# Performance work log

Measured on AMD Instinct MI355X. Metric: run time of the kernel, lower is better.

The kernel has to match this reference:

```python
import jax, jax.numpy as jnp
import numpy as np

D = 64; H = 8; HD = 8; L = 3; FFN = 256
MAX_CHUNKS = 1024; MCL = 16


def rms_norm(x, w, eps=1e-6):
    return x * w * jax.lax.rsqrt(jnp.mean(x * x, axis=-1, keepdims=True) + eps)


def rope(x):
    # x: [B, S, H, HD]
    S, hd = x.shape[1], x.shape[-1]
    half = hd // 2
    freqs = 1.0 / (10000.0 ** (jnp.arange(half, dtype=x.dtype) * 2.0 / hd))
    ang = jnp.arange(S, dtype=x.dtype)[:, None] * freqs  # [S, half]
    cos = jnp.cos(ang)[None, :, None, :]
    sin = jnp.sin(ang)[None, :, None, :]
    x1, x2 = x[..., :half], x[..., half:]
    return jnp.concatenate([x1 * cos - x2 * sin, x1 * sin + x2 * cos], axis=-1)


def block(x, wq, wk, wv, wo, g1, g2, w1, w2):
    B, S, _ = x.shape
    h = rms_norm(x, g1)
    q = rope((h @ wq).reshape(B, S, H, HD))
    k = rope((h @ wk).reshape(B, S, H, HD))
    v = (h @ wv).reshape(B, S, H, HD)
    scores = jnp.einsum('bqhd,bkhd->bhqk', q, k) / jnp.sqrt(jnp.asarray(HD, x.dtype))
    causal = jnp.tril(jnp.ones((S, S), dtype=bool))
    scores = jnp.where(causal, scores, jnp.asarray(-1e30, x.dtype))
    attn = jax.nn.softmax(scores, axis=-1)
    o = jnp.einsum('bhqk,bkhd->bqhd', attn, v).reshape(B, S, D)
    x = x + o @ wo
    h2 = rms_norm(x, g2)
    return x + jax.nn.gelu(h2 @ w1, approximate=False) @ w2


def setup_inputs() -> dict:
    key = jax.random.key(0)
    ks = jax.random.split(key, 12)
    B, S = 4, 2048
    s = 1.0 / np.sqrt(D)
    return {
        'x': jax.random.normal(ks[0], (B, S, D), jnp.float32),
        'pad_token_vector': jax.random.normal(ks[1], (D,), jnp.float32),
        'x_ids': jax.random.randint(ks[2], (B, S), 0, 256),
        'pad_token_id': 257,
        'Wq': jax.random.normal(ks[3], (L, D, D), jnp.float32) * s,
        'Wk': jax.random.normal(ks[4], (L, D, D), jnp.float32) * s,
        'Wv': jax.random.normal(ks[5], (L, D, D), jnp.float32) * s,
        'Wo': jax.random.normal(ks[6], (L, D, D), jnp.float32) * s,
        'ln1': jnp.ones((L, D), jnp.float32),
        'ln2': jnp.ones((L, D), jnp.float32),
        'W1': jax.random.normal(ks[7], (L, D, FFN), jnp.float32) * s,
        'W2': jax.random.normal(ks[8], (L, FFN, D), jnp.float32) * (1.0 / np.sqrt(FFN)),
        'Whead': jax.random.normal(ks[9], (D, 2), jnp.float32) * s,
        'bhead': jnp.zeros((2,), jnp.float32),
    }


def reference(x, pad_token_vector, x_ids, pad_token_id, Wq, Wk, Wv, Wo, ln1, ln2, W1, W2, Whead, bhead):
    B, S, _ = x.shape
    h = x
    for l in range(L):
        h = block(h, Wq[l], Wk[l], Wv[l], Wo[l], ln1[l], ln2[l], W1[l], W2[l])
    logits = h @ Whead + bhead  # [B, S, 2]
    end_mask = logits[..., 0] > logits[..., 1]  # [B, S]
    t = jnp.arange(S)
    # fallback: if a row has no end, mark the last position as an end
    has_end = jnp.any(end_mask, axis=-1, keepdims=True)
    end_mask = jnp.where(has_end, end_mask, t[None, :] == S - 1)
    em = end_mask.astype(jnp.int32)
    num_ends = jnp.sum(em, axis=-1)                 # [B] = number of chunks
    chunk_id = jnp.cumsum(em, axis=-1) - em         # exclusive count of prior ends
    prev_end = jnp.concatenate([jnp.ones((B, 1), bool), end_mask[:, :-1]], axis=1)
    start_marker = jnp.where(prev_end, t[None, :], -1)
    start = jax.lax.associative_scan(jnp.maximum, start_marker, axis=-1)  # cummax -> chunk start per token
    pos = t[None, :] - start                        # position within chunk
    valid = (chunk_id < num_ends[:, None]) & (chunk_id < MAX_CHUNKS) & (pos < MCL)
    c_idx = jnp.where(valid, chunk_id, MAX_CHUNKS)  # invalid -> dummy chunk, sliced off
    p_idx = jnp.where(valid, pos, 0)
    b_idx = jnp.arange(B)[:, None]
    out = jnp.broadcast_to(pad_token_vector, (B, MAX_CHUNKS + 1, MCL, D))
    out = out.at[b_idx, c_idx, p_idx].set(h)[:, :MAX_CHUNKS]
    ids = jnp.full((B, MAX_CHUNKS + 1, MCL), pad_token_id, dtype=x_ids.dtype)
    ids = ids.at[b_idx, c_idx, p_idx].set(x_ids)[:, :MAX_CHUNKS]
    reg_term = jnp.mean(logits[..., 1])
    return out, ids, reg_term
```

## Files before the change

kernel.cpp:

```cpp
#include <hip/hip_runtime.h>
#include <math.h>

constexpr int D   = 64;
constexpr int H   = 8;
constexpr int HD  = 8;
constexpr int NL  = 3;
constexpr int FFNx= 256;
constexpr int Bb  = 4;
constexpr int Ss  = 2048;
constexpr int NT  = Bb * Ss;
constexpr int MAXC= 1024;
constexpr int MCL = 16;

constexpr int TPB  = 72;
constexpr int BPB  = 36;
constexpr int PBSZ = 2304;

constexpr size_t WX  = 0;
constexpr size_t WQ  = 524288;
constexpr size_t WKV = 2621440;
constexpr size_t WPB = 4194304;
constexpr size_t WL1 = 9764864;
constexpr size_t WEM = WL1 + NT;
constexpr size_t WINV= WEM + NT;
constexpr size_t WCT = WINV + Bb*MAXC*MCL;
constexpr size_t WST = WCT + Ss*4;

constexpr float LOG2E = 1.4426950408889634f;

typedef float v2f  __attribute__((ext_vector_type(2)));
typedef float f16v __attribute__((ext_vector_type(16)));
using ckv_t = const __attribute__((address_space(4))) f16v*;

__device__ __forceinline__ float rdlane(float v, int l) {
    return __builtin_bit_cast(float, __builtin_amdgcn_readlane(__builtin_bit_cast(int, v), l));
}

__global__ void k_init(const float* __restrict__ x, float* __restrict__ X,
                       float* __restrict__ ct, float* __restrict__ st) {
    int i = blockIdx.x * blockDim.x + threadIdx.x;
    constexpr int N4 = NT * D / 4;
    if (i < N4) ((float4*)X)[i] = ((const float4*)x)[i];
    if (i < Ss * 4) {
        int s = i >> 2, f = i & 3;
        const float fr[4] = {1.0f, 0.1f, 0.01f, 0.001f};
        float ang = (float)s * fr[f];
        ct[i] = cosf(ang);
        st[i] = sinf(ang);
    }
}

__global__ __launch_bounds__(256) void k_qkv(
    const float* __restrict__ X, const float* __restrict__ Wq,
    const float* __restrict__ Wk, const float* __restrict__ Wv,
    const float* __restrict__ g1, const float* __restrict__ ct,
    const float* __restrict__ st, float* __restrict__ Q,
    float* __restrict__ KV) {
    __shared__ float wq_s[D*D], wk_s[D*D], wv_s[D*D];
    __shared__ float g_s[D];
    int tid = threadIdx.x;
    for (int i = tid; i < D*D; i += 256) {
        wq_s[i] = Wq[i]; wk_s[i] = Wk[i]; wv_s[i] = Wv[i];
    }
    if (tid < D) g_s[tid] = g1[tid];
    __syncthreads();
    int w = tid >> 6, d = tid & 63;
    int t0 = blockIdx.x * 16;
    for (int it = 0; it < 4; ++it) {
        int t = t0 + it*4 + w;
        float xv = X[t*D + d];
        float ss = xv * xv;
        #pragma unroll
        for (int off = 32; off; off >>= 1) ss += __shfl_xor(ss, off);
        float r = 1.0f / sqrtf(ss * (1.0f/D) + 1e-6f);
        float h = xv * g_s[d] * r;
        float aq = 0.f, ak = 0.f, av = 0.f;
        #pragma unroll
        for (int j = 0; j < D; ++j) {
            float hj = rdlane(h, j);
            aq += hj * wq_s[j*D + d];
            ak += hj * wk_s[j*D + d];
            av += hj * wv_s[j*D + d];
        }
        int s  = t & (Ss - 1);
        int e  = d & 7;
        int fi = e & 3;
        float c  = ct[s*4 + fi];
        float sn = st[s*4 + fi];
        float pq = __shfl_xor(aq, 4);
        float pk = __shfl_xor(ak, 4);
        float rq, rk;
        if (e < 4) { rq = aq*c - pq*sn; rk = ak*c - pk*sn; }
        else       { rq = pq*sn + aq*c; rk = pk*sn + ak*c; }
        Q[t*D + d] = rq;
        int bq = t >> 11;
        int hh = d >> 3;
        float* kvp = KV + ((((size_t)(bq*H + hh))*Ss + s) << 4);
        kvp[e]     = rk;
        kvp[8 + e] = av;
    }
}

template<int DIAG>
__device__ __forceinline__ void attn_loop4(
    ckv_t kvs, int L, int rel0,
    const v2f* __restrict__ qp0, const v2f* __restrict__ qp1,
    v2f& l0, v2f& l1, v2f* __restrict__ o0, v2f* __restrict__ o1) {
    #pragma unroll 4
    for (int j = 0; j < 64; ++j) {
        f16v kv = kvs[j];
        v2f a1;
        a1  = qp1[0] * (v2f){kv[0], kv[0]};
        a1 += qp1[1] * (v2f){kv[1], kv[1]};
        a1 += qp1[2] * (v2f){kv[2], kv[2]};
        a1 += qp1[3] * (v2f){kv[3], kv[3]};
        a1 += qp1[4] * (v2f){kv[4], kv[4]};
        a1 += qp1[5] * (v2f){kv[5], kv[5]};
        a1 += qp1[6] * (v2f){kv[6], kv[6]};
        a1 += qp1[7] * (v2f){kv[7], kv[7]};
        if (DIAG == 2) {
            int rel = rel0 + j;
            if (rel > L)      a1.x = -1e30f;
            if (rel > L + 64) a1.y = -1e30f;
        }
        v2f p1;
        p1.x = __builtin_amdgcn_exp2f(a1.x);
        p1.y = __builtin_amdgcn_exp2f(a1.y);
        l1 += p1;
        o1[0] += p1 * (v2f){kv[8],  kv[8]};
        o1[1] += p1 * (v2f){kv[9],  kv[9]};
        o1[2] += p1 * (v2f){kv[10], kv[10]};
        o1[3] += p1 * (v2f){kv[11], kv[11]};
        o1[4] += p1 * (v2f){kv[12], kv[12]};
        o1[5] += p1 * (v2f){kv[13], kv[13]};
        o1[6] += p1 * (v2f){kv[14], kv[14]};
        o1[7] += p1 * (v2f){kv[15], kv[15]};
        if (DIAG != 2) {
            v2f a0;
            a0  = qp0[0] * (v2f){kv[0], kv[0]};
            a0 += qp0[1] * (v2f){kv[1], kv[1]};
            a0 += qp0[2] * (v2f){kv[2], kv[2]};
            a0 += qp0[3] * (v2f){kv[3], kv[3]};
            a0 += qp0[4] * (v2f){kv[4], kv[4]};
            a0 += qp0[5] * (v2f){kv[5], kv[5]};
            a0 += qp0[6] * (v2f){kv[6], kv[6]};
            a0 += qp0[7] * (v2f){kv[7], kv[7]};
            if (DIAG == 1) {
                int rel = rel0 + j;
                if (rel > L)      a0.x = -1e30f;
                if (rel > L + 64) a0.y = -1e30f;
            }
            v2f p0;
            p0.x = __builtin_amdgcn_exp2f(a0.x);
            p0.y = __builtin_amdgcn_exp2f(a0.y);
            l0 += p0;
            o0[0] += p0 * (v2f){kv[8],  kv[8]};
            o0[1] += p0 * (v2f){kv[9],  kv[9]};
            o0[2] += p0 * (v2f){kv[10], kv[10]};
            o0[3] += p0 * (v2f){kv[11], kv[11]};
            o0[4] += p0 * (v2f){kv[12], kv[12]};
            o0[5] += p0 * (v2f){kv[13], kv[13]};
            o0[6] += p0 * (v2f){kv[14], kv[14]};
            o0[7] += p0 * (v2f){kv[15], kv[15]};
        }
    }
}

__global__ __launch_bounds__(256) void k_attn2(
    const float* __restrict__ Qg, const float* __restrict__ KV,
    float* __restrict__ PB) {
    __shared__ float comb[2][PBSZ];
    int xcd  = blockIdx.x & 7;
    int slot = blockIdx.x >> 3;
    int bhg  = slot / BPB;
    int blk  = slot - bhg * BPB;
    int bh   = bhg * 8 + xcd;
    int wvu  = __builtin_amdgcn_readfirstlane(threadIdx.x >> 6);
    int pair = wvu >> 1;
    int half = wvu & 1;
    int widb = blk * 2 + pair;
    int L = threadIdx.x & 63;
    int rem = widb;
    int s = 0;
    while (rem >= 8 - (s >> 1)) { rem -= 8 - (s >> 1); ++s; }
    int t = (s >> 1) + rem;
    int b = bh >> 3, h = bh & 7;
    int qmin = t * 256;
    int k0 = s * 128 + half * 64;

    const float SC = 0.35355339059327373f * LOG2E;
    const float* qp = Qg + ((size_t)(b*Ss + qmin + L))*D + h*HD;
    float4 qa0 = *(const float4*)(qp);
    float4 qb0 = *(const float4*)(qp + 4);
    float4 qa1 = *(const float4*)(qp + 64*D);
    float4 qb1 = *(const float4*)(qp + 64*D + 4);
    float4 qa2 = *(const float4*)(qp + 128*D);
    float4 qb2 = *(const float4*)(qp + 128*D + 4);
    float4 qa3 = *(const float4*)(qp + 192*D);
    float4 qb3 = *(const float4*)(qp + 192*D + 4);
    v2f qp0[8], qp1[8];
    qp0[0] = (v2f){qa0.x*SC, qa1.x*SC};  qp1[0] = (v2f){qa2.x*SC, qa3.x*SC};
    qp0[1] = (v2f){qa0.y*SC, qa1.y*SC};  qp1[1] = (v2f){qa2.y*SC, qa3.y*SC};
    qp0[2] = (v2f){qa0.z*SC, qa1.z*SC};  qp1[2] = (v2f){qa2.z*SC, qa3.z*SC};
    qp0[3] = (v2f){qa0.w*SC, qa1.w*SC};  qp1[3] = (v2f){qa2.w*SC, qa3.w*SC};
    qp0[4] = (v2f){qb0.x*SC, qb1.x*SC};  qp1[4] = (v2f){qb2.x*SC, qb3.x*SC};
    qp0[5] = (v2f){qb0.y*SC, qb1.y*SC};  qp1[5] = (v2f){qb2.y*SC, qb3.y*SC};
    qp0[6] = (v2f){qb0.z*SC, qb1.z*SC};  qp1[6] = (v2f){qb2.z*SC, qb3.z*SC};
    qp0[7] = (v2f){qb0.w*SC, qb1.w*SC};  qp1[7] = (v2f){qb2.w*SC, qb3.w*SC};

    v2f l0 = (v2f){0.f, 0.f}, l1 = (v2f){0.f, 0.f};
    v2f o0[8], o1[8];
    #pragma unroll
    for (int e = 0; e < 8; ++e) { o0[e] = (v2f){0.f, 0.f}; o1[e] = (v2f){0.f, 0.f}; }

    ckv_t kvs = (ckv_t)(unsigned long long)(KV + (((size_t)bh*Ss + k0) << 4));
    if (s == 2*t)          attn_loop4<1>(kvs, L, half*64, qp0, qp1, l0, l1, o0, o1);
    else if (s == 2*t + 1) attn_loop4<2>(kvs, L, half*64, qp0, qp1, l0, l1, o0, o1);
    else                   attn_loop4<0>(kvs, L, half*64, qp0, qp1, l0, l1, o0, o1);

    if (half == 1) {
        comb[pair][L]       = l0.x;
        comb[pair][64 + L]  = l0.y;
        comb[pair][128 + L] = l1.x;
        comb[pair][192 + L] = l1.y;
        #pragma unroll
        for (int e = 0; e < 8; ++e) {
            comb[pair][256 + e*256 + L]       = o0[e].x;
            comb[pair][256 + e*256 + 64 + L]  = o0[e].y;
            comb[pair][256 + e*256 + 128 + L] = o1[e].x;
            comb[pair][256 + e*256 + 192 + L] = o1[e].y;
        }
    }
    __syncthreads();
    if (half == 0) {
        int pbidx = t*(t+1) + s;
        float* pb = PB + ((size_t)bh * TPB + pbidx) * PBSZ;
        pb[L]       = l0.x + comb[pair][L];
        pb[64 + L]  = l0.y + comb[pair][64 + L];
        pb[128 + L] = l1.x + comb[pair][128 + L];
        pb[192 + L] = l1.y + comb[pair][192 + L];
        #pragma unroll
        for (int e = 0; e < 8; ++e) {
            pb[256 + e*256 + L]       = o0[e].x + comb[pair][256 + e*256 + L];
            pb[256 + e*256 + 64 + L]  = o0[e].y + comb[pair][256 + e*256 + 64 + L];
            pb[256 + e*256 + 128 + L] = o1[e].x + comb[pair][256 + e*256 + 128 + L];
            pb[256 + e*256 + 192 + L] = o1[e].y + comb[pair][256 + e*256 + 192 + L];
        }
    }
}

__global__ __launch_bounds__(256) void k_combo(
    const float* __restrict__ PB, float* __restrict__ X,
    const float* __restrict__ Wo) {
    __shared__ float wo_s[D*D];
    __shared__ float oT[32][65];
    int tid = threadIdx.x;
    int seg = blockIdx.x & 7;
    int t   = (blockIdx.x >> 3) & 7;
    int b   = blockIdx.x >> 6;
    for (int i = tid; i < D*D; i += 256) wo_s[i] = Wo[i];

    int h  = tid >> 5;
    int ql = tid & 31;
    int qs = seg*32 + ql;
    int bh = b*8 + h;
    int nch = 2*(t+1);
    float Lx = 0.f;
    float O[8] = {0,0,0,0,0,0,0,0};
    for (int s3 = 0; s3 < nch; ++s3) {
        int idx = t*(t+1) + s3;
        const float* pb = PB + (size_t)(bh*TPB + idx) * PBSZ;
        Lx += pb[qs];
        #pragma unroll
        for (int e = 0; e < 8; ++e) O[e] += pb[256 + e*256 + qs];
    }
    float inv = 1.0f / Lx;
    #pragma unroll
    for (int e = 0; e < 8; ++e) oT[ql][h*8 + e] = O[e] * inv;
    __syncthreads();

    int d = tid & 63, wv = tid >> 6;
    #pragma unroll 2
    for (int k = 0; k < 8; ++k) {
        int tt = wv*8 + k;
        float a = 0.f;
        #pragma unroll
        for (int j = 0; j < D; ++j) a += oT[tt][j] * wo_s[j*D + d];
        X[((size_t)(b*Ss) + t*256 + seg*32 + tt)*D + d] += a;
    }
}

template<bool HEAD>
__global__ __launch_bounds__(256) void k_ffn(
    float* __restrict__ X, const float* __restrict__ g2,
    const float* __restrict__ W1, const float* __restrict__ W2,
    const float* __restrict__ Wh, const float* __restrict__ bhp,
    float* __restrict__ logit1, int* __restrict__ em) {
    __shared__ __align__(16) float h2t[64][20];
    __shared__ float part[16][16];
    __shared__ float g_s[D];
    __shared__ __align__(16) float ult[FFNx][20];
    __shared__ float red[4][16][D];
    int tid = threadIdx.x;
    if (tid < D) g_s[tid] = g2[tid];
    int t0 = blockIdx.x * 16;
    int tk = tid >> 4, li = tid & 15;
    float x0 = X[(t0+tk)*D + li];
    float x1 = X[(t0+tk)*D + li + 16];
    float x2 = X[(t0+tk)*D + li + 32];
    float x3 = X[(t0+tk)*D + li + 48];
    part[tk][li] = x0*x0 + x1*x1 + x2*x2 + x3*x3;
    __syncthreads();
    if (tid < 16) {
        float s = 0.f;
        #pragma unroll
        for (int i = 0; i < 16; ++i) s += part[tid][i];
        part[tid][0] = 1.0f / sqrtf(s * (1.0f/D) + 1e-6f);
    }
    __syncthreads();
    float r = part[tk][0];
    h2t[li][tk]      = x0 * g_s[li]      * r;
    h2t[li + 16][tk] = x1 * g_s[li + 16] * r;
    h2t[li + 32][tk] = x2 * g_s[li + 32] * r;
    h2t[li + 48][tk] = x3 * g_s[li + 48] * r;
    __syncthreads();
    {
        int f = tid;
        v2f acc2[8];
        #pragma unroll
        for (int i = 0; i < 8; ++i) acc2[i] = (v2f){0.f, 0.f};
        for (int j = 0; j < D; ++j) {
            float wv = W1[j*FFNx + f];
            v2f wv2 = (v2f){wv, wv};
            const float4* hp = (const float4*)&h2t[j][0];
            float4 a0 = hp[0], a1 = hp[1], a2 = hp[2], a3 = hp[3];
            const v2f* a0v = (const v2f*)&a0;
            const v2f* a1v = (const v2f*)&a1;
            const v2f* a2v = (const v2f*)&a2;
            const v2f* a3v = (const v2f*)&a3;
            acc2[0] += a0v[0]*wv2;  acc2[1] += a0v[1]*wv2;
            acc2[2] += a1v[0]*wv2;  acc2[3] += a1v[1]*wv2;
            acc2[4] += a2v[0]*wv2;  acc2[5] += a2v[1]*wv2;
            acc2[6] += a3v[0]*wv2;  acc2[7] += a3v[1]*wv2;
        }
        #pragma unroll
        for (int i = 0; i < 8; ++i) {
            float ua = acc2[i].x;
            float ub = acc2[i].y;
            ua = 0.5f * ua * (1.0f + erff(ua * 0.70710678118654752f));
            ub = 0.5f * ub * (1.0f + erff(ub * 0.70710678118654752f));
            ult[f][2*i]     = ua;
            ult[f][2*i + 1] = ub;
        }
    }
    __syncthreads();
    {
        int d = tid & 63, fp = tid >> 6;
        v2f acc2[8];
        #pragma unroll
        for (int i = 0; i < 8; ++i) acc2[i] = (v2f){0.f, 0.f};
        for (int fo = 0; fo < 64; ++fo) {
            int f = fp*64 + fo;
            float wv = W2[f*D + d];
            v2f wv2 = (v2f){wv, wv};
            const float4* up = (const float4*)&ult[f][0];
            float4 u0 = up[0], u1 = up[1], u2 = up[2], u3 = up[3];
            const v2f* u0v = (const v2f*)&u0;
            const v2f* u1v = (const v2f*)&u1;
            const v2f* u2v = (const v2f*)&u2;
            const v2f* u3v = (const v2f*)&u3;
            acc2[0] += u0v[0]*wv2;  acc2[1] += u0v[1]*wv2;
            acc2[2] += u1v[0]*wv2;  acc2[3] += u1v[1]*wv2;
            acc2[4] += u2v[0]*wv2;  acc2[5] += u2v[1]*wv2;
            acc2[6] += u3v[0]*wv2;  acc2[7] += u3v[1]*wv2;
        }
        #pragma unroll
        for (int i = 0; i < 8; ++i) {
            red[fp][2*i][d]     = acc2[i].x;
            red[fp][2*i + 1][d] = acc2[i].y;
        }
        __syncthreads();
        int tk2 = tid >> 6;
        #pragma unroll
        for (int k = 0; k < 4; ++k) {
            int tt = tk2 + k*4;
            float sum = red[0][tt][d] + red[1][tt][d] + red[2][tt][d] + red[3][tt][d];
            float xf = X[(t0 + tt)*D + d] + sum;
            X[(t0 + tt)*D + d] = xf;
            if (HEAD) {
                float p0 = xf * Wh[d*2];
                float p1 = xf * Wh[d*2 + 1];
                #pragma unroll
                for (int off = 32; off; off >>= 1) {
                    p0 += __shfl_xor(p0, off);
                    p1 += __shfl_xor(p1, off);
                }
                if (d == 0) {
                    float l0 = p0 + bhp[0], l1 = p1 + bhp[1];
                    em[t0 + tt] = (l0 > l1) ? 1 : 0;
                    logit1[t0 + tt] = l1;
                }
            }
        }
    }
}

__global__ __launch_bounds__(256) void k_scanreg(
    const int* __restrict__ em, int* __restrict__ inv,
    const float* __restrict__ logit1, float* __restrict__ outreg) {
    __shared__ int ssum[256], smax[256];
    __shared__ int sany, stot;
    int tid = threadIdx.x;
    if (blockIdx.x == Bb) {
        __shared__ float redf[256];
        float s = 0.f;
        for (int i = tid; i < NT; i += 256) s += logit1[i];
        redf[tid] = s;
        __syncthreads();
        for (int off = 128; off; off >>= 1) {
            if (tid < off) redf[tid] += redf[tid + off];
            __syncthreads();
        }
        if (tid == 0) *outreg = redf[0] * (1.0f / NT);
        return;
    }
    int b = blockIdx.x;
    int* invb = inv + b * (MAXC*MCL);
    for (int i = tid; i < MAXC*MCL; i += 256) invb[i] = -1;
    __syncthreads();
    const int* e = em + b*Ss;
    int base = tid * 8;
    int loc[8];
    int lsum = 0, lor = 0;
    #pragma unroll
    for (int i = 0; i < 8; ++i) { loc[i] = e[base + i]; lsum += loc[i]; lor |= loc[i]; }
    ssum[tid] = lor;
    __syncthreads();
    if (tid == 0) { int a = 0; for (int i = 0; i < 256; ++i) a |= ssum[i]; sany = a; }
    __syncthreads();
    int any = sany;
    __syncthreads();
    if (!any && tid == 255) { loc[7] = 1; lsum = 1; }
    int prev = (tid == 0) ? 1 : e[base - 1];
    if (!any && tid) prev = 0;
    int mk[8];
    int lmax = -1;
    #pragma unroll
    for (int i = 0; i < 8; ++i) {
        int pe = (i == 0) ? prev : loc[i - 1];
        if (i == 7 && !any && tid == 255) pe = e[base + 6];
        mk[i] = pe ? (base + i) : -1;
        lmax = max(lmax, mk[i]);
    }
    ssum[tid] = lsum; smax[tid] = lmax;
    __syncthreads();
    if (tid == 0) {
        int rs = 0, rm = -1;
        for (int i = 0; i < 256; ++i) {
            int ts = ssum[i], tm = smax[i];
            ssum[i] = rs; smax[i] = rm;
            rs += ts; rm = max(rm, tm);
        }
        stot = rs;
    }
    __syncthreads();
    int run = ssum[tid], rmax = smax[tid], tot = stot;
    #pragma unroll
    for (int i = 0; i < 8; ++i) {
        int s = base + i;
        rmax = max(rmax, mk[i]);
        int chunk = run;
        run += loc[i];
        int pos = s - rmax;
        bool valid = (chunk < tot) && (chunk < MAXC) && (pos < MCL);
        if (valid) invb[chunk * MCL + pos] = b*Ss + s;
    }
}

__global__ __launch_bounds__(256) void k_out(
    const float* __restrict__ X, const float* __restrict__ pad,
    const int* __restrict__ xids, const int* __restrict__ padid,
    const int* __restrict__ inv, float* __restrict__ out) {
    int i = blockIdx.x * blockDim.x + threadIdx.x;
    constexpr int NV4 = Bb * MAXC * MCL * D / 4;
    constexpr int NI4 = Bb * MAXC * MCL / 4;
    if (i < NV4) {
        int slot = i >> 4;
        int d4 = i & 15;
        int t = inv[slot];
        float4 v = (t >= 0) ? ((const float4*)X)[t*16 + d4]
                            : ((const float4*)pad)[d4];
        ((float4*)out)[i] = v;
    } else if (i < NV4 + NI4) {
        int j = i - NV4;
        float pv = (float)(*padid);
        int base = j * 4;
        int t0_ = inv[base], t1_ = inv[base+1], t2_ = inv[base+2], t3_ = inv[base+3];
        float4 v;
        v.x = (t0_ >= 0) ? (float)xids[t0_] : pv;
        v.y = (t1_ >= 0) ? (float)xids[t1_] : pv;
        v.z = (t2_ >= 0) ? (float)xids[t2_] : pv;
        v.w = (t3_ >= 0) ? (float)xids[t3_] : pv;
        ((float4*)out)[i] = v;
    }
}

extern "C" void kernel_launch(void* const* d_in, const int* in_sizes, int n_in,
                              void* d_out, int out_size, void* d_ws, size_t ws_size,
                              hipStream_t stream) {
    const float* x    = (const float*)d_in[0];
    const float* pad  = (const float*)d_in[1];
    const int*   xids = (const int*)  d_in[2];
    const int*   padid= (const int*)  d_in[3];
    const float* Wq   = (const float*)d_in[4];
    const float* Wk   = (const float*)d_in[5];
    const float* Wv   = (const float*)d_in[6];
    const float* Wo   = (const float*)d_in[7];
    const float* ln1  = (const float*)d_in[8];
    const float* ln2  = (const float*)d_in[9];
    const float* W1   = (const float*)d_in[10];
    const float* W2   = (const float*)d_in[11];
    const float* Wh   = (const float*)d_in[12];
    const float* bh   = (const float*)d_in[13];
    float* out = (float*)d_out;
    float* ws  = (float*)d_ws;

    float* X  = ws + WX;
    float* Qb = ws + WQ;
    float* KVb= ws + WKV;
    float* PBb= ws + WPB;
    float* L1b= ws + WL1;
    int*   EMb= (int*)(ws + WEM);
    int*   INVb=(int*)(ws + WINV);
    float* ct = ws + WCT;
    float* st = ws + WST;

    k_init<<<2048, 256, 0, stream>>>(x, X, ct, st);
    for (int l = 0; l < NL; ++l) {
        k_qkv <<<512, 256, 0, stream>>>(X, Wq + l*D*D, Wk + l*D*D, Wv + l*D*D,
                                        ln1 + l*D, ct, st, Qb, KVb);
        k_attn2<<<32*BPB, 256, 0, stream>>>(Qb, KVb, PBb);
        k_combo<<<256, 256, 0, stream>>>(PBb, X, Wo + l*D*D);
        if (l == NL - 1)
            k_ffn<true ><<<NT/16, 256, 0, stream>>>(X, ln2 + l*D, W1 + l*D*FFNx,
                                                    W2 + l*FFNx*D, Wh, bh, L1b, EMb);
        else
            k_ffn<false><<<NT/16, 256, 0, stream>>>(X, ln2 + l*D, W1 + l*D*FFNx,
                                                    W2 + l*FFNx*D, nullptr, nullptr,
                                                    nullptr, nullptr);
    }
    k_scanreg<<<Bb + 1, 256, 0, stream>>>(EMb, INVb, L1b,
                                          out + (size_t)Bb*MAXC*MCL*D + Bb*MAXC*MCL);
    k_out <<<(Bb*MAXC*MCL*D/4 + Bb*MAXC*MCL/4 + 255)/256, 256, 0, stream>>>(
        X, pad, xids, padid, INVb, out);
}
```

Baseline: 273.8 us.

## Fuse attention partial combine and output projection into the FFN kernel

Merges k_combo (combining the partial attention blocks, normalising, and applying Wo plus the residual) into the FFN kernel. Each block now handles 16 tokens and keeps the updated residual in shared memory, so X is not written and then re-read between the two stages, and one launch per layer goes away. In exchange every block of the 512 reloads the full Wo matrix (previously 256 blocks did), and shared-memory use per block grows, which may lower occupancy.

```diff
diff --git a/kernel.cpp b/kernel.cpp
--- a/kernel.cpp
+++ b/kernel.cpp
@@ -249,66 +249,69 @@
     }
 }
 
-__global__ __launch_bounds__(256) void k_combo(
+template<bool HEAD>
+__global__ __launch_bounds__(256) void k_cffn(
     const float* __restrict__ PB, float* __restrict__ X,
-    const float* __restrict__ Wo) {
-    __shared__ float wo_s[D*D];
-    __shared__ float oT[32][65];
-    int tid = threadIdx.x;
-    int seg = blockIdx.x & 7;
-    int t   = (blockIdx.x >> 3) & 7;
-    int b   = blockIdx.x >> 6;
-    for (int i = tid; i < D*D; i += 256) wo_s[i] = Wo[i];
-
-    int h  = tid >> 5;
-    int ql = tid & 31;
-    int qs = seg*32 + ql;
-    int bh = b*8 + h;
-    int nch = 2*(t+1);
-    float Lx = 0.f;
-    float O[8] = {0,0,0,0,0,0,0,0};
-    for (int s3 = 0; s3 < nch; ++s3) {
-        int idx = t*(t+1) + s3;
-        const float* pb = PB + (size_t)(bh*TPB + idx) * PBSZ;
-        Lx += pb[qs];
-        #pragma unroll
-        for (int e = 0; e < 8; ++e) O[e] += pb[256 + e*256 + qs];
-    }
-    float inv = 1.0f / Lx;
-    #pragma unroll
-    for (int e = 0; e < 8; ++e) oT[ql][h*8 + e] = O[e] * inv;
-    __syncthreads();
-
-    int d = tid & 63, wv = tid >> 6;
-    #pragma unroll 2
-    for (int k = 0; k < 8; ++k) {
-        int tt = wv*8 + k;
-        float a = 0.f;
-        #pragma unroll
-        for (int j = 0; j < D; ++j) a += oT[tt][j] * wo_s[j*D + d];
-        X[((size_t)(b*Ss) + t*256 + seg*32 + tt)*D + d] += a;
-    }
-}
-
-template<bool HEAD>
-__global__ __launch_bounds__(256) void k_ffn(
-    float* __restrict__ X, const float* __restrict__ g2,
+    const float* __restrict__ Wo, const float* __restrict__ g2,
     const float* __restrict__ W1, const float* __restrict__ W2,
     const float* __restrict__ Wh, const float* __restrict__ bhp,
     float* __restrict__ logit1, int* __restrict__ em) {
+    __shared__ float wo_s[D*D];
+    __shared__ float oT[16][65];
+    __shared__ float xt[16][65];
     __shared__ __align__(16) float h2t[64][20];
     __shared__ float part[16][16];
     __shared__ float g_s[D];
     __shared__ __align__(16) float ult[FFNx][20];
     __shared__ float red[4][16][D];
     int tid = threadIdx.x;
+    int gb  = blockIdx.x;
+    int b    = gb >> 7;
+    int tile = gb & 127;
+    int t    = tile >> 4;
+    int sq   = (tile & 15) << 4;
+    int tok0 = b*Ss + t*256 + sq;
+    for (int i = tid; i < D*D; i += 256) wo_s[i] = Wo[i];
     if (tid < D) g_s[tid] = g2[tid];
-    int t0 = blockIdx.x * 16;
+
+    {
+        int h  = tid >> 5;
+        int ql = (tid >> 1) & 15;
+        int eh = tid & 1;
+        int qs = sq + ql;
+        int bh = b*8 + h;
+        int nch = 2*(t+1);
+        float Lx = 0.f;
+        float O[4] = {0,0,0,0};
+        for (int s3 = 0; s3 < nch; ++s3) {
+            int idx = t*(t+1) + s3;
+            const float* pb = PB + (size_t)(bh*TPB + idx) * PBSZ;
+            Lx += pb[qs];
+            #pragma unroll
+            for (int e = 0; e < 4; ++e) O[e] += pb[256 + (eh*4 + e)*256 + qs];
+        }
+        float inv = 1.0f / Lx;
+        #pragma unroll
+        for (int e = 0; e < 4; ++e) oT[ql][h*8 + eh*4 + e] = O[e] * inv;
+    }
+    __syncthreads();
+    {
+        int d = tid & 63, wv = tid >> 6;
+        #pragma unroll
+        for (int k = 0; k < 4; ++k) {
+            int tt = wv*4 + k;
+            float a = 0.f;
+            #pragma unroll
+            for (int j = 0; j < D; ++j) a += oT[tt][j] * wo_s[j*D + d];
+            xt[tt][d] = X[(size_t)(tok0 + tt)*D + d] + a;
+        }
+    }
+    __syncthreads();
     int tk = tid >> 4, li = tid & 15;
-    float x0 = X[(t0+tk)*D + li];
-    float x1 = X[(t0+tk)*D + li + 16];
-    float x2 = X[(t0+tk)*D + li + 32];
-    float x3 = X[(t0+tk)*D + li + 48];
+    float x0 = xt[tk][li];
+    float x1 = xt[tk][li + 16];
+    float x2 = xt[tk][li + 32];
+    float x3 = xt[tk][li + 48];
     part[tk][li] = x0*x0 + x1*x1 + x2*x2 + x3*x3;
     __syncthreads();
     if (tid < 16) {
@@ -385,8 +388,8 @@
         for (int k = 0; k < 4; ++k) {
             int tt = tk2 + k*4;
             float sum = red[0][tt][d] + red[1][tt][d] + red[2][tt][d] + red[3][tt][d];
-            float xf = X[(t0 + tt)*D + d] + sum;
-            X[(t0 + tt)*D + d] = xf;
+            float xf = xt[tt][d] + sum;
+            X[(size_t)(tok0 + tt)*D + d] = xf;
             if (HEAD) {
                 float p0 = xf * Wh[d*2];
                 float p1 = xf * Wh[d*2 + 1];
@@ -397,8 +400,8 @@
                 }
                 if (d == 0) {
                     float l0 = p0 + bhp[0], l1 = p1 + bhp[1];
-                    em[t0 + tt] = (l0 > l1) ? 1 : 0;
-                    logit1[t0 + tt] = l1;
+                    em[tok0 + tt] = (l0 > l1) ? 1 : 0;
+                    logit1[tok0 + tt] = l1;
                 }
             }
         }
@@ -540,14 +543,14 @@
         k_qkv <<<512, 256, 0, stream>>>(X, Wq + l*D*D, Wk + l*D*D, Wv + l*D*D,
                                         ln1 + l*D, ct, st, Qb, KVb);
         k_attn2<<<32*BPB, 256, 0, stream>>>(Qb, KVb, PBb);
-        k_combo<<<256, 256, 0, stream>>>(PBb, X, Wo + l*D*D);
         if (l == NL - 1)
-            k_ffn<true ><<<NT/16, 256, 0, stream>>>(X, ln2 + l*D, W1 + l*D*FFNx,
-                                                    W2 + l*FFNx*D, Wh, bh, L1b, EMb);
+            k_cffn<true ><<<512, 256, 0, stream>>>(PBb, X, Wo + l*D*D, ln2 + l*D,
+                                                   W1 + l*D*FFNx, W2 + l*FFNx*D,
+                                                   Wh, bh, L1b, EMb);
         else
-            k_ffn<false><<<NT/16, 256, 0, stream>>>(X, ln2 + l*D, W1 + l*D*FFNx,
-                                                    W2 + l*FFNx*D, nullptr, nullptr,
-                                                    nullptr, nullptr);
+            k_cffn<false><<<512, 256, 0, stream>>>(PBb, X, Wo + l*D*D, ln2 + l*D,
+                                                   W1 + l*D*FFNx, W2 + l*FFNx*D,
+                                                   nullptr, nullptr, nullptr, nullptr);
     }
     k_scanreg<<<Bb + 1, 256, 0, stream>>>(EMb, INVb, L1b,
                                           out + (size_t)Bb*MAXC*MCL*D + Bb*MAXC*MCL);
```

Measured after the change: 248.0 us, median of 2. -9.4%, faster.
